# Performance work log

Measured on AMD Instinct MI355X. Metric: run time of the kernel, lower is better.

Reference implementation:

```python
import jax, jax.numpy as jnp
import numpy as np

N_NODES = 50000
N_EDGES = 800000
IN_DIM = 232
EMB = 300
HID = 2 * EMB
N_LAYERS = 5
BN_EPS = 1e-5


def setup_inputs() -> dict:
    key = jax.random.key(0)
    ks = jax.random.split(key, 12)
    x = jax.random.normal(ks[0], (N_NODES, IN_DIM), dtype=jnp.float32)
    edge_index = jax.random.randint(ks[1], (2, N_EDGES), 0, N_NODES, dtype=jnp.int64)
    edge_attr = jax.random.normal(ks[2], (N_EDGES, 9), dtype=jnp.float32)
    s_in = 1.0 / np.sqrt(IN_DIM)
    s_emb = 1.0 / np.sqrt(EMB)
    s_hid = 1.0 / np.sqrt(HID)
    lin_in_w = jax.random.uniform(ks[3], (IN_DIM, EMB), jnp.float32, -s_in, s_in)
    lin_in_b = jax.random.uniform(ks[4], (EMB,), jnp.float32, -s_in, s_in)
    w1 = jax.random.uniform(ks[5], (N_LAYERS, EMB, HID), jnp.float32, -s_emb, s_emb)
    b1 = jax.random.uniform(ks[6], (N_LAYERS, HID), jnp.float32, -s_emb, s_emb)
    gamma = jnp.ones((N_LAYERS, HID), jnp.float32)
    beta = jnp.zeros((N_LAYERS, HID), jnp.float32)
    w2 = jax.random.uniform(ks[7], (N_LAYERS, HID, EMB), jnp.float32, -s_hid, s_hid)
    b2 = jax.random.uniform(ks[8], (N_LAYERS, EMB), jnp.float32, -s_hid, s_hid)
    return {"x": x, "edge_index": edge_index, "edge_attr": edge_attr,
            "lin_in_w": lin_in_w, "lin_in_b": lin_in_b,
            "w1": w1, "b1": b1, "gamma": gamma, "beta": beta,
            "w2": w2, "b2": b2}


def reference(x, edge_index, edge_attr, lin_in_w, lin_in_b, w1, b1, gamma, beta, w2, b2):
    n = x.shape[0]
    self_loop = jnp.arange(n, dtype=edge_index.dtype)
    src = jnp.concatenate([edge_index[0], self_loop])  # [E+N]
    dst = jnp.concatenate([edge_index[1], self_loop])
    # input layer linear (232 -> emb)
    h = x @ lin_in_w + lin_in_b  # [N, EMB]
    num_layer = w1.shape[0]
    for l in range(num_layer):
        # gather messages at src, scatter-add at dst (GIN aggr='add' with self loops)
        agg = jax.ops.segment_sum(h[src], dst, num_segments=n)  # [N, EMB]
        # MLP: Linear -> BatchNorm1d (train-mode batch stats) -> ReLU -> Linear
        z = agg @ w1[l] + b1[l]  # [N, HID]
        mu = z.mean(axis=0)
        var = z.var(axis=0)  # biased, as torch BatchNorm uses for normalization
        z = (z - mu) * jax.lax.rsqrt(var + BN_EPS) * gamma[l] + beta[l]
        z = jax.nn.relu(z)
        h_new = z @ w2[l] + b2[l]  # [N, EMB]
        # GNN wrapper: relu between layers, none after the last (drop_ratio=0)
        h = h_new if l == num_layer - 1 else jax.nn.relu(h_new)
    return h  # JK='last'
```

## Files before the change

kernel.cpp:

```cpp
#include <hip/hip_runtime.h>
#include <cstdint>
#include <cstddef>

#define NNODES 50000
#define NEDGES 800000
#define IN_DIM 232
#define EMB 300
#define HID 600
#define NLAYERS 5
#define BN_EPS 1e-5f

#define MPAD 50048
#define K0P 256
#define K1P 320
#define K2P 608
#define N0P 384
#define N1P 640
#define MT_TILES 391
#define CSTR 140

typedef unsigned short ushort_t;
typedef __attribute__((ext_vector_type(8))) short bf16x8;
typedef __attribute__((ext_vector_type(4))) float f32x4;

__device__ __forceinline__ float b2f(ushort_t u) {
    unsigned int x = (unsigned int)u << 16;
    return __builtin_bit_cast(float, x);
}
__device__ __forceinline__ ushort_t f2b(float f) {
    unsigned int x = __builtin_bit_cast(unsigned int, f);
    unsigned int r = (x + 0x7fffu + ((x >> 16) & 1u)) >> 16;
    return (ushort_t)r;
}

__device__ __forceinline__ void gl_lds16(const void* gsrc, void* ldst) {
    __builtin_amdgcn_global_load_lds(
        (const __attribute__((address_space(1))) void*)gsrc,
        (__attribute__((address_space(3))) void*)ldst, 16, 0, 0);
}

__global__ void detect_mode_kernel(const unsigned int* __restrict__ ei, int* __restrict__ mode) {
    if (threadIdx.x == 0 && blockIdx.x == 0) {
        int nz = 0;
        for (int i = 0; i < 256; ++i) nz += (ei[2 * i + 1] != 0u);
        *mode = (nz == 0) ? 1 : 0;
    }
}
__device__ __forceinline__ int load_edge(const int* ei, int mode, long long idx) {
    if (mode) return (int)((const long long*)ei)[idx];
    return ei[idx];
}

__global__ void hist_kernel(const int* __restrict__ ei, const int* __restrict__ mode,
                            int* __restrict__ deg) {
    int i = blockIdx.x * blockDim.x + threadIdx.x;
    if (i >= NEDGES) return;
    int d = load_edge(ei, *mode, (long long)NEDGES + i);
    atomicAdd(&deg[d], 1);
}

__global__ void scan_block_sums(const int* __restrict__ deg, int* __restrict__ bsum, int n) {
    __shared__ int s[256];
    int t = threadIdx.x;
    int i = blockIdx.x * 256 + t;
    s[t] = (i < n) ? deg[i] : 0;
    __syncthreads();
    for (int off = 128; off > 0; off >>= 1) {
        if (t < off) s[t] += s[t + off];
        __syncthreads();
    }
    if (t == 0) bsum[blockIdx.x] = s[0];
}
// ... 29 lines not shown
    }
    int excl = s[t] - v + bsum[blockIdx.x];
    if (i < n) {
        offs[i] = excl;
        cursor[i] = excl;
        if (i == n - 1) offs[n] = excl + v;
    }
}

__global__ void fill_csr(const int* __restrict__ ei, const int* __restrict__ mode,
                         int* __restrict__ cursor, int* __restrict__ csr) {
    int i = blockIdx.x * blockDim.x + threadIdx.x;
    if (i >= NEDGES) return;
    int m = *mode;
    int s = load_edge(ei, m, i);
    int d = load_edge(ei, m, (long long)NEDGES + i);
    int p = atomicAdd(&cursor[d], 1);
    csr[p] = s;
}

__global__ void cast_x_kernel(const float* __restrict__ x, ushort_t* __restrict__ o) {
    int idx = blockIdx.x * 256 + threadIdx.x;
    if (idx >= NNODES * K0P) return;
    int row = idx >> 8, k = idx & 255;
    float v = (k < IN_DIM) ? x[(size_t)row * IN_DIM + k] : 0.f;
    o[idx] = f2b(v);
}
__global__ void conv_lin_kernel(const float* __restrict__ w, ushort_t* __restrict__ o) {
    int idx = blockIdx.x * 256 + threadIdx.x;
    if (idx >= N0P * K0P) return;
    int n = idx >> 8, k = idx & 255;
    float v = (n < EMB && k < IN_DIM) ? w[(size_t)k * EMB + n] : 0.f;
    o[idx] = f2b(v);
}
__global__ void conv_w1_kernel(const float* __restrict__ w, ushort_t* __restrict__ o) {
    int idx = blockIdx.x * 256 + threadIdx.x;
    if (idx >= NLAYERS * N1P * K1P) return;
    int l = idx / (N1P * K1P);
    int r = idx - l * (N1P * K1P);
    int n = r / K1P, k = r - n * K1P;
    float v = (n < HID && k < EMB) ? w[((size_t)l * EMB + k) * HID + n] : 0.f;
    o[idx] = f2b(v);
}
__global__ void conv_w2_kernel(const float* __restrict__ w, ushort_t* __restrict__ o) {
    int idx = blockIdx.x * 256 + threadIdx.x;
    if (idx >= NLAYERS * N0P * K2P) return;
    int l = idx / (N0P * K2P);
    int r = idx - l * (N0P * K2P);
    int n = r / K2P, k = r - n * K2P;
    float v = (n < EMB && k < HID) ? w[((size_t)l * HID + k) * EMB + n] : 0.f;
    o[idx] = f2b(v);
}

__global__ __launch_bounds__(256) void aggregate_bf16(
    const ushort_t* __restrict__ h, ushort_t* __restrict__ agg,
    const int* __restrict__ offs, const int* __restrict__ csr) {
    const int w = blockIdx.x * 4 + (threadIdx.x >> 6);
    const int lane = threadIdx.x & 63;
    const int wid0 = w * 2, wid1 = wid0 + 1;
    if (wid0 >= NNODES) return;
    const bool hasb = lane < 11;
    float a0[4], a1[4] = {0.f, 0.f, 0.f, 0.f};
    float c0[4], c1[4] = {0.f, 0.f, 0.f, 0.f};
    {
        const ushort4* r0 = (const ushort4*)(h + (size_t)wid0 * K1P);
        const ushort4* r1 = (const ushort4*)(h + (size_t)wid1 * K1P);
        ushort4 v0 = r0[lane], v1 = r1[lane];
        a0[0] = b2f(v0.x); a0[1] = b2f(v0.y); a0[2] = b2f(v0.z); a0[3] = b2f(v0.w);
        c0[0] = b2f(v1.x); c0[1] = b2f(v1.y); c0[2] = b2f(v1.z); c0[3] = b2f(v1.w);
        if (hasb) {
            ushort4 w0 = r0[64 + lane], w1 = r1[64 + lane];
            a1[0] = b2f(w0.x); a1[1] = b2f(w0.y); a1[2] = b2f(w0.z); a1[3] = b2f(w0.w);
            c1[0] = b2f(w1.x); c1[1] = b2f(w1.y); c1[2] = b2f(w1.z); c1[3] = b2f(w1.w);
        }
    }
    int p0 = offs[wid0], e0 = offs[wid0 + 1];
    int p1 = e0, e1 = offs[wid1 + 1];
    while (p0 < e0 && p1 < e1) {
        const ushort4* r0 = (const ushort4*)(h + (size_t)csr[p0] * K1P); ++p0;
        const ushort4* r1 = (const ushort4*)(h + (size_t)csr[p1] * K1P); ++p1;
        ushort4 v0 = r0[lane];
        ushort4 v1 = r1[lane];
        a0[0] += b2f(v0.x); a0[1] += b2f(v0.y); a0[2] += b2f(v0.z); a0[3] += b2f(v0.w);
        c0[0] += b2f(v1.x); c0[1] += b2f(v1.y); c0[2] += b2f(v1.z); c0[3] += b2f(v1.w);
        if (hasb) {
            ushort4 w0 = r0[64 + lane];
            ushort4 w1 = r1[64 + lane];
            a1[0] += b2f(w0.x); a1[1] += b2f(w0.y); a1[2] += b2f(w0.z); a1[3] += b2f(w0.w);
            c1[0] += b2f(w1.x); c1[1] += b2f(w1.y); c1[2] += b2f(w1.z); c1[3] += b2f(w1.w);
        }
    }
    while (p0 < e0) {
        const ushort4* r0 = (const ushort4*)(h + (size_t)csr[p0] * K1P); ++p0;
        ushort4 v0 = r0[lane];
        a0[0] += b2f(v0.x); a0[1] += b2f(v0.y); a0[2] += b2f(v0.z); a0[3] += b2f(v0.w);
        if (hasb) {
            ushort4 w0 = r0[64 + lane];
            a1[0] += b2f(w0.x); a1[1] += b2f(w0.y); a1[2] += b2f(w0.z); a1[3] += b2f(w0.w);
        }
    }
    while (p1 < e1) {
        const ushort4* r1 = (const ushort4*)(h + (size_t)csr[p1] * K1P); ++p1;
        ushort4 v1 = r1[lane];
        c0[0] += b2f(v1.x); c0[1] += b2f(v1.y); c0[2] += b2f(v1.z); c0[3] += b2f(v1.w);
        if (hasb) {
            ushort4 w1 = r1[64 + lane];
            c1[0] += b2f(w1.x); c1[1] += b2f(w1.y); c1[2] += b2f(w1.z); c1[3] += b2f(w1.w);
        }
    }
    ushort4* o0 = (ushort4*)(agg + (size_t)wid0 * K1P);
    ushort4* o1 = (ushort4*)(agg + (size_t)wid1 * K1P);
    ushort4 ov;
    ov.x = f2b(a0[0]); ov.y = f2b(a0[1]); ov.z = f2b(a0[2]); ov.w = f2b(a0[3]);
    o0[lane] = ov;
    ov.x = f2b(c0[0]); ov.y = f2b(c0[1]); ov.z = f2b(c0[2]); ov.w = f2b(c0[3]);
    o1[lane] = ov;
    if (hasb) {
        ov.x = f2b(a1[0]); ov.y = f2b(a1[1]); ov.z = f2b(a1[2]); ov.w = f2b(a1[3]);
        o0[64 + lane] = ov;
        ov.x = f2b(c1[0]); ov.y = f2b(c1[1]); ov.z = f2b(c1[2]); ov.w = f2b(c1[3]);
        o1[64 + lane] = ov;
    }
    if (lane < 5) {
        ushort4 zz; zz.x = zz.y = zz.z = zz.w = 0;
        o0[75 + lane] = zz;
        o1[75 + lane] = zz;
    }
}

template <int PRO, int RELU, int STATS, int OUT_BF16>
__global__ __launch_bounds__(256) void gemm_mfma(
    const ushort_t* __restrict__ A, int lda,
    const ushort_t* __restrict__ Bt, int ldb,
    const float* __restrict__ bias,
    void* __restrict__ C, int ldc, int M, int N, int K,
    const float* __restrict__ pscale, const float* __restrict__ pshift, int Kreal,
    float* __restrict__ stats, int NB) {
    __shared__ ushort_t sh[17920];
    __shared__ float psS[PRO ? 640 : 4];
    __shared__ float pfS[PRO ? 640 : 4];

    const int bid = blockIdx.x;
    const int xcd = bid & 7, slot = bid >> 3;
    const int mt = (slot / NB) * 8 + xcd;
    if (mt >= MT_TILES) return;
    const int nt = slot % NB;
    const int m0 = mt << 7, n0 = nt << 7;

    const int tid = threadIdx.x;
    const int wave = tid >> 6, lane = tid & 63;
    const int wm = wave >> 1, wn = wave & 1;
    const int NT = K >> 5;

    const int srow = lane >> 2;
    const int schunk = ((lane & 3) ^ ((lane >> 3) & 3)) << 3;
    const ushort_t* bP = Bt + (size_t)(n0 + (wave << 5) + srow) * ldb + schunk;
    const ushort_t* aPg = A + (size_t)(m0 + (wave << 5) + srow) * lda + schunk;
    const ushort_t* aPr = A + (size_t)(m0 + (wave << 5) + srow) * lda + ((lane & 3) << 3);
    const int a16 = lda << 4, b16 = ldb << 4;
    const int ldsW = wave << 10;
    ushort_t* const AS0 = sh;
    ushort_t* const AS1 = sh + 4096;
    ushort_t* const BS0 = sh + 8192;
    ushort_t* const BS1 = sh + 12288;

    const int fr = lane & 15, fq = lane >> 4;
    const int rdoff = (fq ^ ((fr >> 1) & 3)) << 3;

    f32x4 acc[4][4];
#pragma unroll
    for (int i = 0; i < 4; ++i)
#pragma unroll
        for (int j = 0; j < 4; ++j) acc[i][j] = {0.f, 0.f, 0.f, 0.f};

    if (PRO) {
        for (int i = tid; i < 640; i += 256) {
            psS[i] = (i < Kreal) ? pscale[i] : 0.f;
            pfS[i] = (i < Kreal) ? pshift[i] : 0.f;
        }
        __syncthreads();
    }

    uint4 ar0, ar1;
    const ushort_t* aNext;
    const ushort_t* bNext = bP + 32;
    if (PRO) {
        ar0 = *(const uint4*)aPr;
        ar1 = *(const uint4*)(aPr + a16);
        gl_lds16(bP, BS0 + ldsW);
        gl_lds16(bP + b16, BS0 + ldsW + 512);
        aNext = aPr + 32;
    } else {
        gl_lds16(aPg, AS0 + ldsW);
        gl_lds16(aPg + a16, AS0 + ldsW + 512);
        gl_lds16(bP, BS0 + ldsW);
        gl_lds16(bP + b16, BS0 + ldsW + 512);
        aNext = aPg + 32;
    }

    int cur = 0;
    for (int t = 0; t < NT; ++t) {
        ushort_t* const ASc = cur ? AS1 : AS0;
        ushort_t* const BSc = cur ? BS1 : BS0;
        ushort_t* const ASn = cur ? AS0 : AS1;
        ushort_t* const BSn = cur ? BS0 : BS1;
        if (PRO) {
            asm volatile("s_waitcnt vmcnt(2)" ::: "memory");
            const int kb = (t << 5) + ((lane & 3) << 3);
            float4 psa = *(const float4*)&psS[kb];
            float4 psb = *(const float4*)&psS[kb + 4];
            float4 pfa = *(const float4*)&pfS[kb];
            float4 pfb = *(const float4*)&pfS[kb + 4];
            float ps[8] = {psa.x, psa.y, psa.z, psa.w, psb.x, psb.y, psb.z, psb.w};
            float pf[8] = {pfa.x, pfa.y, pfa.z, pfa.w, pfb.x, pfb.y, pfb.z, pfb.w};
            bf16x8 w0, w1;
            const ushort_t* u0 = (const ushort_t*)&ar0;
            const ushort_t* u1 = (const ushort_t*)&ar1;
#pragma unroll
            for (int j = 0; j < 8; ++j) {
                float v0 = b2f(u0[j]) * ps[j] + pf[j];
                float v1 = b2f(u1[j]) * ps[j] + pf[j];
                w0[j] = (short)f2b(v0 > 0.f ? v0 : 0.f);
                w1[j] = (short)f2b(v1 > 0.f ? v1 : 0.f);
            }
            ushort_t* dA = ASc + ((wave << 5) + srow) * 32 + schunk;
            *(bf16x8*)dA = w0;
            *(bf16x8*)(dA + 16 * 32) = w1;
            if (t + 1 < NT) {
                ar0 = *(const uint4*)aNext;
                ar1 = *(const uint4*)(aNext + a16);
                gl_lds16(bNext, BSn + ldsW);
                gl_lds16(bNext + b16, BSn + ldsW + 512);
                aNext += 32; bNext += 32;
                asm volatile("s_waitcnt vmcnt(4) lgkmcnt(0)" ::: "memory");
            } else {
                asm volatile("s_waitcnt vmcnt(0) lgkmcnt(0)" ::: "memory");
            }
        } else {
            if (t + 1 < NT) {
                gl_lds16(aNext, ASn + ldsW);
                gl_lds16(aNext + a16, ASn + ldsW + 512);
                gl_lds16(bNext, BSn + ldsW);
                gl_lds16(bNext + b16, BSn + ldsW + 512);
                aNext += 32; bNext += 32;
                asm volatile("s_waitcnt vmcnt(4)" ::: "memory");
            } else {
                asm volatile("s_waitcnt vmcnt(0)" ::: "memory");
            }
        }
        __builtin_amdgcn_s_barrier();
        __builtin_amdgcn_sched_barrier(0);

        bf16x8 af[4], bf[4];
#pragma unroll
        for (int mi = 0; mi < 4; ++mi)
            af[mi] = *(const bf16x8*)&ASc[((wm << 6) + (mi << 4) + fr) * 32 + rdoff];
#pragma unroll
        for (int nj = 0; nj < 4; ++nj)
            bf[nj] = *(const bf16x8*)&BSc[((wn << 6) + (nj << 4) + fr) * 32 + rdoff];
#pragma unroll
        for (int mi = 0; mi < 4; ++mi)
#pragma unroll
            for (int nj = 0; nj < 4; ++nj)
                acc[mi][nj] = __builtin_amdgcn_mfma_f32_16x16x32_bf16(af[mi], bf[nj], acc[mi][nj], 0, 0, 0);

        __builtin_amdgcn_sched_barrier(0);
        __builtin_amdgcn_s_barrier();
        cur ^= 1;
    }

    if (STATS) {
        float s1[4] = {0.f, 0.f, 0.f, 0.f}, s2[4] = {0.f, 0.f, 0.f, 0.f};
#pragma unroll
        for (int nj = 0; nj < 4; ++nj) {
            const int col = n0 + (wn << 6) + (nj << 4) + fr;
            if (col < N) {
                const float bv = bias[col];
#pragma unroll
                for (int mi = 0; mi < 4; ++mi) {
                    const int rbase = m0 + (wm << 6) + (mi << 4) + (fq << 2);
#pragma unroll
                    for (int r = 0; r < 4; ++r) {
                        if (rbase + r < M) {
                            float v = acc[mi][nj][r] + bv;
                            if (RELU) v = v > 0.f ? v : 0.f;
                            s1[nj] += v; s2[nj] += v * v;
                        }
                    }
                }
            }
        }
#pragma unroll
        for (int nj = 0; nj < 4; ++nj) {
            s1[nj] += __shfl_xor(s1[nj], 16);
            s1[nj] += __shfl_xor(s1[nj], 32);
            s2[nj] += __shfl_xor(s2[nj], 16);
            s2[nj] += __shfl_xor(s2[nj], 32);
        }
        if (lane < 16) {
#pragma unroll
            for (int nj = 0; nj < 4; ++nj) {
                const int col = n0 + (wn << 6) + (nj << 4) + lane;
                if (col < N) {
                    atomicAdd(&stats[col], s1[nj]);
                    atomicAdd(&stats[N + col], s2[nj]);
                }
            }
        }
    }

    if (OUT_BF16) {
        ushort_t* ct = sh;
#pragma unroll
        for (int nj = 0; nj < 4; ++nj) {
            const int col_l = (wn << 6) + (nj << 4) + fr;
            const int col = n0 + col_l;
            const float bv = (col < N) ? bias[col] : 0.f;
#pragma unroll
            for (int mi = 0; mi < 4; ++mi) {
                const int rl0 = (wm << 6) + (mi << 4) + (fq << 2);
#pragma unroll
                for (int r = 0; r < 4; ++r) {
                    float v = acc[mi][nj][r] + bv;
                    if (RELU) v = v > 0.f ? v : 0.f;
                    ct[(rl0 + r) * CSTR + col_l] = f2b(v);
                }
            }
        }
        __syncthreads();
        const int rr = tid >> 1, half = tid & 1;
        const int grow = m0 + rr;
        if (grow < M) {
            const ushort_t* src = ct + rr * CSTR + (half << 6);
            ushort_t* dst = (ushort_t*)C + (size_t)grow * ldc + n0 + (half << 6);
#pragma unroll
            for (int c = 0; c < 8; ++c) {
                const int gc = n0 + (half << 6) + (c << 3);
                if (gc + 7 < N) {
                    uint2 u0 = *(const uint2*)(src + (c << 3));
                    uint2 u1 = *(const uint2*)(src + (c << 3) + 4);
                    uint4 o; o.x = u0.x; o.y = u0.y; o.z = u1.x; o.w = u1.y;
                    *(uint4*)(dst + (c << 3)) = o;
                } else {
                    for (int j = 0; j < 8; ++j)
                        if (gc + j < N) dst[(c << 3) + j] = src[(c << 3) + j];
                }
            }
        }
    } else {
        float* ctf = (float*)sh;
#pragma unroll
        for (int ph = 0; ph < 2; ++ph) {
            if (wm == ph) {
#pragma unroll
                for (int nj = 0; nj < 4; ++nj) {
                    const int col_l = (wn << 6) + (nj << 4) + fr;
                    const int col = n0 + col_l;
                    const float bv = (col < N) ? bias[col] : 0.f;
#pragma unroll
                    for (int mi = 0; mi < 4; ++mi) {
                        const int rl0 = (mi << 4) + (fq << 2);
#pragma unroll
                        for (int r = 0; r < 4; ++r) {
                            float v = acc[mi][nj][r] + bv;
                            if (RELU) v = v > 0.f ? v : 0.f;
                            ctf[(rl0 + r) * CSTR + col_l] = v;
                        }
                    }
                }
            }
            __syncthreads();
            const int rr = tid >> 2, q = tid & 3;
            const int grow = m0 + (ph << 6) + rr;
            if (grow < M) {
                const float* src = ctf + rr * CSTR + (q << 5);
                float* dst = (float*)C + (size_t)grow * ldc + n0 + (q << 5);
#pragma unroll
                for (int c = 0; c < 8; ++c) {
                    const int gc = n0 + (q << 5) + (c << 2);
                    if (gc + 3 < N) {
                        *(float4*)(dst + (c << 2)) = *(const float4*)(src + (c << 2));
                    } else {
                        for (int j = 0; j < 4; ++j)
                            if (gc + j < N) dst[(c << 2) + j] = src[(c << 2) + j];
                    }
                }
            }
            __syncthreads();
        }
    }
}

__global__ void bn_finalize(const float* __restrict__ stats, const float* __restrict__ gamma,
                            const float* __restrict__ beta, float* __restrict__ pscale,
                            float* __restrict__ pshift, int N, float invM) {
    int c = blockIdx.x * blockDim.x + threadIdx.x;
    if (c >= N) return;
    float mu = stats[c] * invM;
    float var = stats[N + c] * invM - mu * mu;
    float rs = rsqrtf(var + BN_EPS);
    float g = gamma[c] * rs;
    pscale[c] = g;
    pshift[c] = beta[c] - mu * g;
}

extern "C" void kernel_launch(void* const* d_in, const int* in_sizes, int n_in,
                              void* d_out, int out_size, void* d_ws, size_t ws_size,
                              hipStream_t stream) {
    const float* x = (const float*)d_in[0];
    const int* ei = (const int*)d_in[1];
    const float* lin_in_w = (const float*)d_in[3];
    const float* lin_in_b = (const float*)d_in[4];
    const float* w1 = (const float*)d_in[5];
    const float* b1 = (const float*)d_in[6];
    const float* gamma = (const float*)d_in[7];
    const float* beta = (const float*)d_in[8];
    const float* w2 = (const float*)d_in[9];
    const float* b2 = (const float*)d_in[10];
    float* out = (float*)d_out;

    char* p = (char*)d_ws;
    auto alloc = [&](size_t bytes) {
        char* r = p;
        p += (bytes + 255) & ~(size_t)255;
        return r;
    };
    ushort_t* xb  = (ushort_t*)alloc((size_t)MPAD * K0P * 2);
    ushort_t* h   = (ushort_t*)alloc((size_t)MPAD * K1P * 2);
    ushort_t* agg = (ushort_t*)alloc((size_t)MPAD * K1P * 2);
    ushort_t* z   = (ushort_t*)alloc((size_t)MPAD * K2P * 2);
    ushort_t* lint = (ushort_t*)alloc((size_t)N0P * K0P * 2);
    ushort_t* w1t  = (ushort_t*)alloc((size_t)NLAYERS * N1P * K1P * 2);
    ushort_t* w2t  = (ushort_t*)alloc((size_t)NLAYERS * N0P * K2P * 2);
    int* deg    = (int*)alloc(NNODES * 4);
    int* cursor = (int*)alloc(NNODES * 4);
    int* offs   = (int*)alloc((NNODES + 1) * 4);
    int* bsum   = (int*)alloc(1024);
    int* csr    = (int*)alloc((size_t)NEDGES * 4);
    float* stats  = (float*)alloc((size_t)NLAYERS * 2 * HID * 4);
    float* pscale = (float*)alloc(HID * 4);
    float* pshift = (float*)alloc(HID * 4);
    int* mode   = (int*)alloc(256);
    (void)ws_size; (void)in_sizes; (void)n_in; (void)out_size;

    hipMemsetAsync(deg, 0, NNODES * 4, stream);
    hipMemsetAsync(stats, 0, (size_t)NLAYERS * 2 * HID * 4, stream);

    detect_mode_kernel<<<1, 64, 0, stream>>>((const unsigned int*)ei, mode);
    hist_kernel<<<(NEDGES + 255) / 256, 256, 0, stream>>>(ei, mode, deg);
    const int nb = (NNODES + 255) / 256;
    scan_block_sums<<<nb, 256, 0, stream>>>(deg, bsum, NNODES);
    scan_bsums<<<1, 256, 0, stream>>>(bsum, nb);
    scan_final<<<nb, 256, 0, stream>>>(deg, bsum, offs, cursor, NNODES);
    fill_csr<<<(NEDGES + 255) / 256, 256, 0, stream>>>(ei, mode, cursor, csr);

    cast_x_kernel<<<(NNODES * K0P + 255) / 256, 256, 0, stream>>>(x, xb);
    conv_lin_kernel<<<(N0P * K0P + 255) / 256, 256, 0, stream>>>(lin_in_w, lint);
    conv_w1_kernel<<<(NLAYERS * N1P * K1P + 255) / 256, 256, 0, stream>>>(w1, w1t);
    conv_w2_kernel<<<(NLAYERS * N0P * K2P + 255) / 256, 256, 0, stream>>>(w2, w2t);

    const int G3 = 8 * 49 * 3;
    const int G5 = 8 * 49 * 5;

    gemm_mfma<0, 0, 0, 1><<<G3, 256, 0, stream>>>(
        xb, K0P, lint, K0P, lin_in_b, h, K1P, NNODES, EMB, K0P,
        nullptr, nullptr, 0, nullptr, 3);

    for (int l = 0; l < NLAYERS; ++l) {
        aggregate_bf16<<<(NNODES / 2 + 3) / 4, 256, 0, stream>>>(h, agg, offs, csr);
        gemm_mfma<0, 0, 1, 1><<<G5, 256, 0, stream>>>(
            agg, K1P, w1t + (size_t)l * N1P * K1P, K1P, b1 + (size_t)l * HID,
            z, K2P, NNODES, HID, K1P,
            nullptr, nullptr, 0, stats + (size_t)l * 2 * HID, 5);
        bn_finalize<<<(HID + 255) / 256, 256, 0, stream>>>(
            stats + (size_t)l * 2 * HID, gamma + (size_t)l * HID, beta + (size_t)l * HID,
            pscale, pshift, HID, 1.f / NNODES);
        if (l < NLAYERS - 1) {
            gemm_mfma<1, 1, 0, 1><<<G3, 256, 0, stream>>>(
                z, K2P, w2t + (size_t)l * N0P * K2P, K2P, b2 + (size_t)l * EMB,
                h, K1P, NNODES, EMB, K2P,
                pscale, pshift, HID, nullptr, 3);
        } else {
            gemm_mfma<1, 0, 0, 0><<<G3, 256, 0, stream>>>(
                z, K2P, w2t + (size_t)l * N0P * K2P, K2P, b2 + (size_t)l * EMB,
                out, EMB, NNODES, EMB, K2P,
                pscale, pshift, HID, nullptr, 3);
        }
    }
}
```

Before: 1.183 ms.

## Restructure aggregation into column-chunked node groups with XCD-aware chunk mapping

Replaces the two-nodes-per-wave gather kernel with one that splits the feature columns into 8 chunks, mapped by block index to the 8 XCDs. Within a wave, 6 lane groups of 10 lanes each walk 16 consecutive nodes, loading 8 bytes per lane. A zeroed padding row stands in for inactive lanes so the loop needs no branches. The aim is to keep each XCD's column slice of h resident in its own L2, improving cache reuse on the random gathers. The cost is 4 idle lanes per wave, wave-level divergence from uneven degrees, and an extra memset of the padding rows.

After: 2.928 ms. 148% more time.

```diff
diff --git a/kernel.cpp b/kernel.cpp
--- a/kernel.cpp
+++ b/kernel.cpp
@@ -18,6 +18,10 @@
 #define N1P 640
 #define MT_TILES 391
 #define CSTR 140
+
+#define NPG 16
+#define ZROW 50000
+#define AGG_SLOTS 131
 
 typedef unsigned short ushort_t;
 typedef __attribute__((ext_vector_type(8))) short bf16x8;
@@ -153,79 +157,67 @@
     o[idx] = f2b(v);
 }
 
-__global__ __launch_bounds__(256) void aggregate_bf16(
+__global__ __launch_bounds__(256) void aggregate_cs(
     const ushort_t* __restrict__ h, ushort_t* __restrict__ agg,
     const int* __restrict__ offs, const int* __restrict__ csr) {
-    const int w = blockIdx.x * 4 + (threadIdx.x >> 6);
-    const int lane = threadIdx.x & 63;
-    const int wid0 = w * 2, wid1 = wid0 + 1;
-    if (wid0 >= NNODES) return;
-    const bool hasb = lane < 11;
-    float a0[4], a1[4] = {0.f, 0.f, 0.f, 0.f};
-    float c0[4], c1[4] = {0.f, 0.f, 0.f, 0.f};
-    {
-        const ushort4* r0 = (const ushort4*)(h + (size_t)wid0 * K1P);
-        const ushort4* r1 = (const ushort4*)(h + (size_t)wid1 * K1P);
-        ushort4 v0 = r0[lane], v1 = r1[lane];
-        a0[0] = b2f(v0.x); a0[1] = b2f(v0.y); a0[2] = b2f(v0.z); a0[3] = b2f(v0.w);
-        c0[0] = b2f(v1.x); c0[1] = b2f(v1.y); c0[2] = b2f(v1.z); c0[3] = b2f(v1.w);
-        if (hasb) {
-            ushort4 w0 = r0[64 + lane], w1 = r1[64 + lane];
-            a1[0] = b2f(w0.x); a1[1] = b2f(w0.y); a1[2] = b2f(w0.z); a1[3] = b2f(w0.w);
-            c1[0] = b2f(w1.x); c1[1] = b2f(w1.y); c1[2] = b2f(w1.z); c1[3] = b2f(w1.w);
-        }
-    }
-    int p0 = offs[wid0], e0 = offs[wid0 + 1];
-    int p1 = e0, e1 = offs[wid1 + 1];
-    while (p0 < e0 && p1 < e1) {
-        const ushort4* r0 = (const ushort4*)(h + (size_t)csr[p0] * K1P); ++p0;
-        const ushort4* r1 = (const ushort4*)(h + (size_t)csr[p1] * K1P); ++p1;
-        ushort4 v0 = r0[lane];
-        ushort4 v1 = r1[lane];
-        a0[0] += b2f(v0.x); a0[1] += b2f(v0.y); a0[2] += b2f(v0.z); a0[3] += b2f(v0.w);
-        c0[0] += b2f(v1.x); c0[1] += b2f(v1.y); c0[2] += b2f(v1.z); c0[3] += b2f(v1.w);
-        if (hasb) {
-            ushort4 w0 = r0[64 + lane];
-            ushort4 w1 = r1[64 + lane];
-            a1[0] += b2f(w0.x); a1[1] += b2f(w0.y); a1[2] += b2f(w0.z); a1[3] += b2f(w0.w);
-            c1[0] += b2f(w1.x); c1[1] += b2f(w1.y); c1[2] += b2f(w1.z); c1[3] += b2f(w1.w);
-        }
-    }
-    while (p0 < e0) {
-        const ushort4* r0 = (const ushort4*)(h + (size_t)csr[p0] * K1P); ++p0;
-        ushort4 v0 = r0[lane];
-        a0[0] += b2f(v0.x); a0[1] += b2f(v0.y); a0[2] += b2f(v0.z); a0[3] += b2f(v0.w);
-        if (hasb) {
-            ushort4 w0 = r0[64 + lane];
-            a1[0] += b2f(w0.x); a1[1] += b2f(w0.y); a1[2] += b2f(w0.z); a1[3] += b2f(w0.w);
-        }
-    }
-    while (p1 < e1) {
-        const ushort4* r1 = (const ushort4*)(h + (size_t)csr[p1] * K1P); ++p1;
-        ushort4 v1 = r1[lane];
-        c0[0] += b2f(v1.x); c0[1] += b2f(v1.y); c0[2] += b2f(v1.z); c0[3] += b2f(v1.w);
-        if (hasb) {
-            ushort4 w1 = r1[64 + lane];
-            c1[0] += b2f(w1.x); c1[1] += b2f(w1.y); c1[2] += b2f(w1.z); c1[3] += b2f(w1.w);
-        }
-    }
-    ushort4* o0 = (ushort4*)(agg + (size_t)wid0 * K1P);
-    ushort4* o1 = (ushort4*)(agg + (size_t)wid1 * K1P);
-    ushort4 ov;
-    ov.x = f2b(a0[0]); ov.y = f2b(a0[1]); ov.z = f2b(a0[2]); ov.w = f2b(a0[3]);
-    o0[lane] = ov;
-    ov.x = f2b(c0[0]); ov.y = f2b(c0[1]); ov.z = f2b(c0[2]); ov.w = f2b(c0[3]);
-    o1[lane] = ov;
-    if (hasb) {
-        ov.x = f2b(a1[0]); ov.y = f2b(a1[1]); ov.z = f2b(a1[2]); ov.w = f2b(a1[3]);
-        o0[64 + lane] = ov;
-        ov.x = f2b(c1[0]); ov.y = f2b(c1[1]); ov.z = f2b(c1[2]); ov.w = f2b(c1[3]);
-        o1[64 + lane] = ov;
-    }
-    if (lane < 5) {
-        ushort4 zz; zz.x = zz.y = zz.z = zz.w = 0;
-        o0[75 + lane] = zz;
-        o1[75 + lane] = zz;
+    const int chunk = blockIdx.x & 7;
+    const int slot = blockIdx.x >> 3;
+    const int wave = threadIdx.x >> 6, lane = threadIdx.x & 63;
+    const int g = lane / 10;
+    const int cl = lane - g * 10;
+    const bool real = (g < 6);
+    const int gid = (slot * 4 + wave) * 6 + g;
+    int v = real ? gid * NPG : NNODES;
+    int vend = real ? (gid * NPG + NPG) : NNODES;
+    if (vend > NNODES) vend = NNODES;
+    if (v > NNODES) v = NNODES;
+    const int colu = chunk * 20 + cl * 2;
+    const unsigned int* __restrict__ h32 = (const unsigned int*)h;
+    unsigned int* __restrict__ a32 = (unsigned int*)agg;
+
+    int beg = 0, end = 0, e = 0;
+    if (v < vend) {
+        beg = __builtin_nontemporal_load(offs + v);
+        end = __builtin_nontemporal_load(offs + v + 1);
+        e = beg - 1;
+    }
+    float a0 = 0.f, a1 = 0.f, a2 = 0.f, a3 = 0.f;
+
+    while (__any(v < vend)) {
+        const bool self = e < beg;
+        const bool active = (e < end) & (v < vend);
+        int ci = self ? 0 : e;
+        ci = (ci < NEDGES) ? ci : 0;
+        const int csrv = __builtin_nontemporal_load(csr + ci);
+        int src = self ? v : csrv;
+        src = active ? src : ZROW;
+        const unsigned long long L =
+            *(const unsigned long long*)(h32 + (unsigned int)src * (K1P / 2) + colu);
+        const unsigned int lo = (unsigned int)L;
+        const unsigned int hi = (unsigned int)(L >> 32);
+        a0 += __builtin_bit_cast(float, lo << 16);
+        a1 += __builtin_bit_cast(float, lo & 0xffff0000u);
+        a2 += __builtin_bit_cast(float, hi << 16);
+        a3 += __builtin_bit_cast(float, hi & 0xffff0000u);
+        e += active ? 1 : 0;
+        const bool done = (e >= end) & (v < vend);
+        if (__any(done)) {
+            if (done) {
+                unsigned int p0 = (unsigned int)f2b(a0) | ((unsigned int)f2b(a1) << 16);
+                unsigned int p1 = (unsigned int)f2b(a2) | ((unsigned int)f2b(a3) << 16);
+                if (colu * 2 >= 300) { p0 = 0u; p1 = 0u; }
+                const unsigned long long P = (unsigned long long)p0 | ((unsigned long long)p1 << 32);
+                __builtin_nontemporal_store(
+                    P, (unsigned long long*)(a32 + (unsigned int)v * (K1P / 2) + colu));
+                ++v;
+                a0 = a1 = a2 = a3 = 0.f;
+                if (v < vend) {
+                    beg = __builtin_nontemporal_load(offs + v);
+                    end = __builtin_nontemporal_load(offs + v + 1);
+                    e = beg - 1;
+                }
+            }
+        }
     }
 }
 
@@ -546,6 +538,7 @@
 
     hipMemsetAsync(deg, 0, NNODES * 4, stream);
     hipMemsetAsync(stats, 0, (size_t)NLAYERS * 2 * HID * 4, stream);
+    hipMemsetAsync(h + (size_t)NNODES * K1P, 0, (size_t)(MPAD - NNODES) * K1P * 2, stream);
 
     detect_mode_kernel<<<1, 64, 0, stream>>>((const unsigned int*)ei, mode);
     hist_kernel<<<(NEDGES + 255) / 256, 256, 0, stream>>>(ei, mode, deg);
@@ -568,7 +561,7 @@
         nullptr, nullptr, 0, nullptr, 3);
 
     for (int l = 0; l < NLAYERS; ++l) {
-        aggregate_bf16<<<(NNODES / 2 + 3) / 4, 256, 0, stream>>>(h, agg, offs, csr);
+        aggregate_cs<<<AGG_SLOTS * 8, 256, 0, stream>>>(h, agg, offs, csr);
         gemm_mfma<0, 0, 1, 1><<<G5, 256, 0, stream>>>(
             agg, K1P, w1t + (size_t)l * N1P * K1P, K1P, b1 + (size_t)l * HID,
             z, K2P, NNODES, HID, K1P,
```

## Enlarge GEMM tiles to 256 rows with 512 threads and widen aggregation to four nodes per wave

Applied to the files above, without the earlier changes.

The MFMA GEMM now uses 512-thread blocks computing 256x128 tiles, so each B tile loaded into LDS is shared across twice as many rows. The epilogue is restructured into multi-pass LDS staging, and MPAD is raised to cover 256-row tiles. The aggregation kernel now processes four destination nodes per wave in lockstep. Exhausted neighbor lists redirect to a zeroed padding row rather than branching, and loads and stores use nontemporal hints. The trade-off is more LDS and register pressure per block, plus wasted loads on the padding row when node degrees are imbalanced.

Result: slower. 1.638 ms (+38.5%).

```diff
diff --git a/kernel.cpp b/kernel.cpp
--- a/kernel.cpp
+++ b/kernel.cpp
@@ -10,14 +10,15 @@
 #define NLAYERS 5
 #define BN_EPS 1e-5f
 
-#define MPAD 50048
+#define MPAD 50176
 #define K0P 256
 #define K1P 320
 #define K2P 608
 #define N0P 384
 #define N1P 640
-#define MT_TILES 391
-#define CSTR 140
+#define MT_TILES 196
+#define CSTR 144
+#define ZROW 50000
 
 typedef unsigned short ushort_t;
 typedef __attribute__((ext_vector_type(8))) short bf16x8;
@@ -158,86 +159,71 @@
     const int* __restrict__ offs, const int* __restrict__ csr) {
     const int w = blockIdx.x * 4 + (threadIdx.x >> 6);
     const int lane = threadIdx.x & 63;
-    const int wid0 = w * 2, wid1 = wid0 + 1;
-    if (wid0 >= NNODES) return;
+    const int v0 = w * 4;
+    if (v0 >= NNODES) return;
     const bool hasb = lane < 11;
-    float a0[4], a1[4] = {0.f, 0.f, 0.f, 0.f};
-    float c0[4], c1[4] = {0.f, 0.f, 0.f, 0.f};
-    {
-        const ushort4* r0 = (const ushort4*)(h + (size_t)wid0 * K1P);
-        const ushort4* r1 = (const ushort4*)(h + (size_t)wid1 * K1P);
-        ushort4 v0 = r0[lane], v1 = r1[lane];
-        a0[0] = b2f(v0.x); a0[1] = b2f(v0.y); a0[2] = b2f(v0.z); a0[3] = b2f(v0.w);
-        c0[0] = b2f(v1.x); c0[1] = b2f(v1.y); c0[2] = b2f(v1.z); c0[3] = b2f(v1.w);
+    float ac[4][8];
+    int pc[4], ec[4];
+#pragma unroll
+    for (int c = 0; c < 4; ++c) {
+        pc[c] = __builtin_nontemporal_load(offs + v0 + c);
+        ec[c] = __builtin_nontemporal_load(offs + v0 + c + 1);
+        const ushort4* r = (const ushort4*)(h + (size_t)(v0 + c) * K1P);
+        ushort4 x = r[lane];
+        ac[c][0] = b2f(x.x); ac[c][1] = b2f(x.y); ac[c][2] = b2f(x.z); ac[c][3] = b2f(x.w);
+        ac[c][4] = 0.f; ac[c][5] = 0.f; ac[c][6] = 0.f; ac[c][7] = 0.f;
         if (hasb) {
-            ushort4 w0 = r0[64 + lane], w1 = r1[64 + lane];
-            a1[0] = b2f(w0.x); a1[1] = b2f(w0.y); a1[2] = b2f(w0.z); a1[3] = b2f(w0.w);
-            c1[0] = b2f(w1.x); c1[1] = b2f(w1.y); c1[2] = b2f(w1.z); c1[3] = b2f(w1.w);
-        }
-    }
-    int p0 = offs[wid0], e0 = offs[wid0 + 1];
-    int p1 = e0, e1 = offs[wid1 + 1];
-    while (p0 < e0 && p1 < e1) {
-        const ushort4* r0 = (const ushort4*)(h + (size_t)csr[p0] * K1P); ++p0;
-        const ushort4* r1 = (const ushort4*)(h + (size_t)csr[p1] * K1P); ++p1;
-        ushort4 v0 = r0[lane];
-        ushort4 v1 = r1[lane];
-        a0[0] += b2f(v0.x); a0[1] += b2f(v0.y); a0[2] += b2f(v0.z); a0[3] += b2f(v0.w);
-        c0[0] += b2f(v1.x); c0[1] += b2f(v1.y); c0[2] += b2f(v1.z); c0[3] += b2f(v1.w);
+            ushort4 y = r[64 + lane];
+            ac[c][4] = b2f(y.x); ac[c][5] = b2f(y.y); ac[c][6] = b2f(y.z); ac[c][7] = b2f(y.w);
+        }
+    }
+    while ((pc[0] < ec[0]) | (pc[1] < ec[1]) | (pc[2] < ec[2]) | (pc[3] < ec[3])) {
+        int src[4];
+#pragma unroll
+        for (int c = 0; c < 4; ++c) {
+            const bool a = pc[c] < ec[c];
+            const int idx = a ? pc[c] : 0;
+            const int s = __builtin_nontemporal_load(csr + idx);
+            src[c] = a ? s : ZROW;
+            pc[c] += a ? 1 : 0;
+        }
+#pragma unroll
+        for (int c = 0; c < 4; ++c) {
+            const ushort4* r = (const ushort4*)(h + (size_t)src[c] * K1P);
+            ushort4 x = r[lane];
+            ac[c][0] += b2f(x.x); ac[c][1] += b2f(x.y); ac[c][2] += b2f(x.z); ac[c][3] += b2f(x.w);
+            if (hasb) {
+                ushort4 y = r[64 + lane];
+                ac[c][4] += b2f(y.x); ac[c][5] += b2f(y.y); ac[c][6] += b2f(y.z); ac[c][7] += b2f(y.w);
+            }
+        }
+    }
+#pragma unroll
+    for (int c = 0; c < 4; ++c) {
+        unsigned long long* o = (unsigned long long*)(agg + (size_t)(v0 + c) * K1P);
+        unsigned long long P =
+            (unsigned long long)((unsigned int)f2b(ac[c][0]) | ((unsigned int)f2b(ac[c][1]) << 16)) |
+            ((unsigned long long)((unsigned int)f2b(ac[c][2]) | ((unsigned int)f2b(ac[c][3]) << 16)) << 32);
+        __builtin_nontemporal_store(P, o + lane);
         if (hasb) {
-            ushort4 w0 = r0[64 + lane];
-            ushort4 w1 = r1[64 + lane];
-            a1[0] += b2f(w0.x); a1[1] += b2f(w0.y); a1[2] += b2f(w0.z); a1[3] += b2f(w0.w);
-            c1[0] += b2f(w1.x); c1[1] += b2f(w1.y); c1[2] += b2f(w1.z); c1[3] += b2f(w1.w);
-        }
-    }
-    while (p0 < e0) {
-        const ushort4* r0 = (const ushort4*)(h + (size_t)csr[p0] * K1P); ++p0;
-        ushort4 v0 = r0[lane];
-        a0[0] += b2f(v0.x); a0[1] += b2f(v0.y); a0[2] += b2f(v0.z); a0[3] += b2f(v0.w);
-        if (hasb) {
-            ushort4 w0 = r0[64 + lane];
-            a1[0] += b2f(w0.x); a1[1] += b2f(w0.y); a1[2] += b2f(w0.z); a1[3] += b2f(w0.w);
-        }
-    }
-    while (p1 < e1) {
-        const ushort4* r1 = (const ushort4*)(h + (size_t)csr[p1] * K1P); ++p1;
-        ushort4 v1 = r1[lane];
-        c0[0] += b2f(v1.x); c0[1] += b2f(v1.y); c0[2] += b2f(v1.z); c0[3] += b2f(v1.w);
-        if (hasb) {
-            ushort4 w1 = r1[64 + lane];
-            c1[0] += b2f(w1.x); c1[1] += b2f(w1.y); c1[2] += b2f(w1.z); c1[3] += b2f(w1.w);
-        }
-    }
-    ushort4* o0 = (ushort4*)(agg + (size_t)wid0 * K1P);
-    ushort4* o1 = (ushort4*)(agg + (size_t)wid1 * K1P);
-    ushort4 ov;
-    ov.x = f2b(a0[0]); ov.y = f2b(a0[1]); ov.z = f2b(a0[2]); ov.w = f2b(a0[3]);
-    o0[lane] = ov;
-    ov.x = f2b(c0[0]); ov.y = f2b(c0[1]); ov.z = f2b(c0[2]); ov.w = f2b(c0[3]);
-    o1[lane] = ov;
-    if (hasb) {
-        ov.x = f2b(a1[0]); ov.y = f2b(a1[1]); ov.z = f2b(a1[2]); ov.w = f2b(a1[3]);
-        o0[64 + lane] = ov;
-        ov.x = f2b(c1[0]); ov.y = f2b(c1[1]); ov.z = f2b(c1[2]); ov.w = f2b(c1[3]);
-        o1[64 + lane] = ov;
-    }
-    if (lane < 5) {
-        ushort4 zz; zz.x = zz.y = zz.z = zz.w = 0;
-        o0[75 + lane] = zz;
-        o1[75 + lane] = zz;
+            unsigned long long Q =
+                (unsigned long long)((unsigned int)f2b(ac[c][4]) | ((unsigned int)f2b(ac[c][5]) << 16)) |
+                ((unsigned long long)((unsigned int)f2b(ac[c][6]) | ((unsigned int)f2b(ac[c][7]) << 16)) << 32);
+            __builtin_nontemporal_store(Q, o + 64 + lane);
+        }
+        if (lane < 5) __builtin_nontemporal_store(0ull, o + 75 + lane);
     }
 }
 
 template <int PRO, int RELU, int STATS, int OUT_BF16>
-__global__ __launch_bounds__(256) void gemm_mfma(
+__global__ __launch_bounds__(512, 4) void gemm_mfma(
     const ushort_t* __restrict__ A, int lda,
     const ushort_t* __restrict__ Bt, int ldb,
     const float* __restrict__ bias,
     void* __restrict__ C, int ldc, int M, int N, int K,
     const float* __restrict__ pscale, const float* __restrict__ pshift, int Kreal,
     float* __restrict__ stats, int NB) {
-    __shared__ ushort_t sh[17920];
+    __shared__ ushort_t sh[24576];
     __shared__ float psS[PRO ? 640 : 4];
     __shared__ float pfS[PRO ? 640 : 4];
 
@@ -246,7 +232,7 @@
     const int mt = (slot / NB) * 8 + xcd;
     if (mt >= MT_TILES) return;
     const int nt = slot % NB;
-    const int m0 = mt << 7, n0 = nt << 7;
+    const int m0 = mt << 8, n0 = nt << 7;
 
     const int tid = threadIdx.x;
     const int wave = tid >> 6, lane = tid & 63;
@@ -255,15 +241,16 @@
 
     const int srow = lane >> 2;
     const int schunk = ((lane & 3) ^ ((lane >> 3) & 3)) << 3;
-    const ushort_t* bP = Bt + (size_t)(n0 + (wave << 5) + srow) * ldb + schunk;
+    const ushort_t* bP = Bt + (size_t)(n0 + (wave << 4) + srow) * ldb + schunk;
     const ushort_t* aPg = A + (size_t)(m0 + (wave << 5) + srow) * lda + schunk;
     const ushort_t* aPr = A + (size_t)(m0 + (wave << 5) + srow) * lda + ((lane & 3) << 3);
-    const int a16 = lda << 4, b16 = ldb << 4;
-    const int ldsW = wave << 10;
+    const int a16 = lda << 4;
+    const int aW = wave << 10;
+    const int bW = wave << 9;
     ushort_t* const AS0 = sh;
-    ushort_t* const AS1 = sh + 4096;
-    ushort_t* const BS0 = sh + 8192;
-    ushort_t* const BS1 = sh + 12288;
+    ushort_t* const AS1 = sh + 8192;
+    ushort_t* const BS0 = sh + 16384;
+    ushort_t* const BS1 = sh + 20480;
 
     const int fr = lane & 15, fq = lane >> 4;
     const int rdoff = (fq ^ ((fr >> 1) & 3)) << 3;
@@ -275,7 +262,7 @@
         for (int j = 0; j < 4; ++j) acc[i][j] = {0.f, 0.f, 0.f, 0.f};
 
     if (PRO) {
-        for (int i = tid; i < 640; i += 256) {
+        for (int i = tid; i < 640; i += 512) {
             psS[i] = (i < Kreal) ? pscale[i] : 0.f;
             pfS[i] = (i < Kreal) ? pshift[i] : 0.f;
         }
@@ -288,14 +275,12 @@
     if (PRO) {
         ar0 = *(const uint4*)aPr;
         ar1 = *(const uint4*)(aPr + a16);
-        gl_lds16(bP, BS0 + ldsW);
-        gl_lds16(bP + b16, BS0 + ldsW + 512);
+        gl_lds16(bP, BS0 + bW);
         aNext = aPr + 32;
     } else {
-        gl_lds16(aPg, AS0 + ldsW);
-        gl_lds16(aPg + a16, AS0 + ldsW + 512);
-        gl_lds16(bP, BS0 + ldsW);
-        gl_lds16(bP + b16, BS0 + ldsW + 512);
+        gl_lds16(aPg, AS0 + aW);
+        gl_lds16(aPg + a16, AS0 + aW + 512);
+        gl_lds16(bP, BS0 + bW);
         aNext = aPg + 32;
     }
 
@@ -306,7 +291,7 @@
         ushort_t* const ASn = cur ? AS0 : AS1;
         ushort_t* const BSn = cur ? BS0 : BS1;
         if (PRO) {
-            asm volatile("s_waitcnt vmcnt(2)" ::: "memory");
+            asm volatile("s_waitcnt vmcnt(1)" ::: "memory");
             const int kb = (t << 5) + ((lane & 3) << 3);
             float4 psa = *(const float4*)&psS[kb];
             float4 psb = *(const float4*)&psS[kb + 4];
@@ -326,25 +311,23 @@
             }
             ushort_t* dA = ASc + ((wave << 5) + srow) * 32 + schunk;
             *(bf16x8*)dA = w0;
-            *(bf16x8*)(dA + 16 * 32) = w1;
+            *(bf16x8*)(dA + 512) = w1;
             if (t + 1 < NT) {
                 ar0 = *(const uint4*)aNext;
                 ar1 = *(const uint4*)(aNext + a16);
-                gl_lds16(bNext, BSn + ldsW);
-                gl_lds16(bNext + b16, BSn + ldsW + 512);
+                gl_lds16(bNext, BSn + bW);
                 aNext += 32; bNext += 32;
-                asm volatile("s_waitcnt vmcnt(4) lgkmcnt(0)" ::: "memory");
+                asm volatile("s_waitcnt vmcnt(3) lgkmcnt(0)" ::: "memory");
             } else {
                 asm volatile("s_waitcnt vmcnt(0) lgkmcnt(0)" ::: "memory");
             }
         } else {
             if (t + 1 < NT) {
-                gl_lds16(aNext, ASn + ldsW);
-                gl_lds16(aNext + a16, ASn + ldsW + 512);
-                gl_lds16(bNext, BSn + ldsW);
-                gl_lds16(bNext + b16, BSn + ldsW + 512);
+                gl_lds16(aNext, ASn + aW);
+                gl_lds16(aNext + a16, ASn + aW + 512);
+                gl_lds16(bNext, BSn + bW);
                 aNext += 32; bNext += 32;
-                asm volatile("s_waitcnt vmcnt(4)" ::: "memory");
+                asm volatile("s_waitcnt vmcnt(3)" ::: "memory");
             } else {
                 asm volatile("s_waitcnt vmcnt(0)" ::: "memory");
             }
@@ -413,46 +396,49 @@
     if (OUT_BF16) {
         ushort_t* ct = sh;
 #pragma unroll
-        for (int nj = 0; nj < 4; ++nj) {
-            const int col_l = (wn << 6) + (nj << 4) + fr;
-            const int col = n0 + col_l;
-            const float bv = (col < N) ? bias[col] : 0.f;
-#pragma unroll
-            for (int mi = 0; mi < 4; ++mi) {
-                const int rl0 = (wm << 6) + (mi << 4) + (fq << 2);
-#pragma unroll
-                for (int r = 0; r < 4; ++r) {
-                    float v = acc[mi][nj][r] + bv;
-                    if (RELU) v = v > 0.f ? v : 0.f;
-                    ct[(rl0 + r) * CSTR + col_l] = f2b(v);
+        for (int p = 0; p < 2; ++p) {
+            if ((wm >> 1) == p) {
+#pragma unroll
+                for (int nj = 0; nj < 4; ++nj) {
+                    const int col_l = (wn << 6) + (nj << 4) + fr;
+                    const int col = n0 + col_l;
+                    const float bv = (col < N) ? bias[col] : 0.f;
+#pragma unroll
+                    for (int mi = 0; mi < 4; ++mi) {
+                        const int rl0 = ((wm & 1) << 6) + (mi << 4) + (fq << 2);
+#pragma unroll
+                        for (int r = 0; r < 4; ++r) {
+                            float v = acc[mi][nj][r] + bv;
+                            if (RELU) v = v > 0.f ? v : 0.f;
+                            ct[(rl0 + r) * CSTR + col_l] = f2b(v);
+                        }
+                    }
                 }
             }
-        }
-        __syncthreads();
-        const int rr = tid >> 1, half = tid & 1;
-        const int grow = m0 + rr;
-        if (grow < M) {
-            const ushort_t* src = ct + rr * CSTR + (half << 6);
-            ushort_t* dst = (ushort_t*)C + (size_t)grow * ldc + n0 + (half << 6);
-#pragma unroll
-            for (int c = 0; c < 8; ++c) {
-                const int gc = n0 + (half << 6) + (c << 3);
-                if (gc + 7 < N) {
-                    uint2 u0 = *(const uint2*)(src + (c << 3));
-                    uint2 u1 = *(const uint2*)(src + (c << 3) + 4);
-                    uint4 o; o.x = u0.x; o.y = u0.y; o.z = u1.x; o.w = u1.y;
-                    *(uint4*)(dst + (c << 3)) = o;
-                } else {
-                    for (int j = 0; j < 8; ++j)
-                        if (gc + j < N) dst[(c << 3) + j] = src[(c << 3) + j];
+            __syncthreads();
+            const int rl = tid >> 2, q = tid & 3;
+            const int grow = m0 + (p << 7) + rl;
+            if (grow < M) {
+                const ushort_t* src = ct + rl * CSTR + (q << 5);
+                ushort_t* dst = (ushort_t*)C + (size_t)grow * ldc + n0 + (q << 5);
+#pragma unroll
+                for (int c = 0; c < 4; ++c) {
+                    const int gc = n0 + (q << 5) + (c << 3);
+                    if (gc + 7 < N) {
+                        *(uint4*)(dst + (c << 3)) = *(const uint4*)(src + (c << 3));
+                    } else {
+                        for (int j = 0; j < 8; ++j)
+                            if (gc + j < N) dst[(c << 3) + j] = src[(c << 3) + j];
+                    }
                 }
             }
+            __syncthreads();
         }
     } else {
         float* ctf = (float*)sh;
 #pragma unroll
-        for (int ph = 0; ph < 2; ++ph) {
-            if (wm == ph) {
+        for (int p = 0; p < 4; ++p) {
+            if (wm == p) {
 #pragma unroll
                 for (int nj = 0; nj < 4; ++nj) {
                     const int col_l = (wn << 6) + (nj << 4) + fr;
@@ -471,14 +457,14 @@
                 }
             }
             __syncthreads();
-            const int rr = tid >> 2, q = tid & 3;
-            const int grow = m0 + (ph << 6) + rr;
+            const int rl = tid >> 3, q = tid & 7;
+            const int grow = m0 + (p << 6) + rl;
             if (grow < M) {
-                const float* src = ctf + rr * CSTR + (q << 5);
-                float* dst = (float*)C + (size_t)grow * ldc + n0 + (q << 5);
-#pragma unroll
-                for (int c = 0; c < 8; ++c) {
-                    const int gc = n0 + (q << 5) + (c << 2);
+                const float* src = ctf + rl * CSTR + (q << 4);
+                float* dst = (float*)C + (size_t)grow * ldc + n0 + (q << 4);
+#pragma unroll
+                for (int c = 0; c < 4; ++c) {
+                    const int gc = n0 + (q << 4) + (c << 2);
                     if (gc + 3 < N) {
                         *(float4*)(dst + (c << 2)) = *(const float4*)(src + (c << 2));
                     } else {
@@ -546,6 +532,7 @@
 
     hipMemsetAsync(deg, 0, NNODES * 4, stream);
     hipMemsetAsync(stats, 0, (size_t)NLAYERS * 2 * HID * 4, stream);
+    hipMemsetAsync(h + (size_t)NNODES * K1P, 0, (size_t)(MPAD - NNODES) * K1P * 2, stream);
 
     detect_mode_kernel<<<1, 64, 0, stream>>>((const unsigned int*)ei, mode);
     hist_kernel<<<(NEDGES + 255) / 256, 256, 0, stream>>>(ei, mode, deg);
@@ -560,16 +547,16 @@
     conv_w1_kernel<<<(NLAYERS * N1P * K1P + 255) / 256, 256, 0, stream>>>(w1, w1t);
     conv_w2_kernel<<<(NLAYERS * N0P * K2P + 255) / 256, 256, 0, stream>>>(w2, w2t);
 
-    const int G3 = 8 * 49 * 3;
-    const int G5 = 8 * 49 * 5;
-
-    gemm_mfma<0, 0, 0, 1><<<G3, 256, 0, stream>>>(
+    const int G3 = 8 * 25 * 3;
+    const int G5 = 8 * 25 * 5;
+
+    gemm_mfma<0, 0, 0, 1><<<G3, 512, 0, stream>>>(
         xb, K0P, lint, K0P, lin_in_b, h, K1P, NNODES, EMB, K0P,
         nullptr, nullptr, 0, nullptr, 3);
 
     for (int l = 0; l < NLAYERS; ++l) {
-        aggregate_bf16<<<(NNODES / 2 + 3) / 4, 256, 0, stream>>>(h, agg, offs, csr);
-        gemm_mfma<0, 0, 1, 1><<<G5, 256, 0, stream>>>(
+        aggregate_bf16<<<NNODES / 16, 256, 0, stream>>>(h, agg, offs, csr);
+        gemm_mfma<0, 0, 1, 1><<<G5, 512, 0, stream>>>(
             agg, K1P, w1t + (size_t)l * N1P * K1P, K1P, b1 + (size_t)l * HID,
             z, K2P, NNODES, HID, K1P,
             nullptr, nullptr, 0, stats + (size_t)l * 2 * HID, 5);
@@ -577,12 +564,12 @@
             stats + (size_t)l * 2 * HID, gamma + (size_t)l * HID, beta + (size_t)l * HID,
             pscale, pshift, HID, 1.f / NNODES);
         if (l < NLAYERS - 1) {
-            gemm_mfma<1, 1, 0, 1><<<G3, 256, 0, stream>>>(
+            gemm_mfma<1, 1, 0, 1><<<G3, 512, 0, stream>>>(
                 z, K2P, w2t + (size_t)l * N0P * K2P, K2P, b2 + (size_t)l * EMB,
                 h, K1P, NNODES, EMB, K2P,
                 pscale, pshift, HID, nullptr, 3);
         } else {
-            gemm_mfma<1, 0, 0, 0><<<G3, 256, 0, stream>>>(
+            gemm_mfma<1, 0, 0, 0><<<G3, 512, 0, stream>>>(
                 z, K2P, w2t + (size_t)l * N0P * K2P, K2P, b2 + (size_t)l * EMB,
                 out, EMB, NNODES, EMB, K2P,
                 pscale, pshift, HID, nullptr, 3);
```

## Load non-prologue GEMM fragments directly from global into registers, bypassing LDS

Applied to the files above, without the earlier changes.

For GEMMs without a fused prologue, the LDS double-buffered staging is replaced by loading MFMA A/B fragments straight from global memory into registers, using a two-stage software register pipeline. This removes LDS writes and reads plus the block barriers on that path, but each wave now fetches its own fragments, so global and L2 traffic rises because tiles are no longer shared across waves through LDS. A barrier is added before the epilogue's LDS reuse, and the padding rows of h are zeroed so the direct loads read defined data.

Measured after the change: 1.378 ms. +16.5%, slower.

```diff
diff --git a/kernel.cpp b/kernel.cpp
--- a/kernel.cpp
+++ b/kernel.cpp
@@ -253,20 +253,7 @@
     const int wm = wave >> 1, wn = wave & 1;
     const int NT = K >> 5;
 
-    const int srow = lane >> 2;
-    const int schunk = ((lane & 3) ^ ((lane >> 3) & 3)) << 3;
-    const ushort_t* bP = Bt + (size_t)(n0 + (wave << 5) + srow) * ldb + schunk;
-    const ushort_t* aPg = A + (size_t)(m0 + (wave << 5) + srow) * lda + schunk;
-    const ushort_t* aPr = A + (size_t)(m0 + (wave << 5) + srow) * lda + ((lane & 3) << 3);
-    const int a16 = lda << 4, b16 = ldb << 4;
-    const int ldsW = wave << 10;
-    ushort_t* const AS0 = sh;
-    ushort_t* const AS1 = sh + 4096;
-    ushort_t* const BS0 = sh + 8192;
-    ushort_t* const BS1 = sh + 12288;
-
     const int fr = lane & 15, fq = lane >> 4;
-    const int rdoff = (fq ^ ((fr >> 1) & 3)) << 3;
 
     f32x4 acc[4][4];
 #pragma unroll
@@ -274,38 +261,97 @@
 #pragma unroll
         for (int j = 0; j < 4; ++j) acc[i][j] = {0.f, 0.f, 0.f, 0.f};
 
-    if (PRO) {
+    if (!PRO) {
+        const ushort_t* aB[4];
+        const ushort_t* bB[4];
+#pragma unroll
+        for (int mi = 0; mi < 4; ++mi)
+            aB[mi] = A + (size_t)(m0 + (wm << 6) + (mi << 4) + fr) * lda + (fq << 3);
+#pragma unroll
+        for (int nj = 0; nj < 4; ++nj)
+            bB[nj] = Bt + (size_t)(n0 + (wn << 6) + (nj << 4) + fr) * ldb + (fq << 3);
+
+        uint4 a0[4], b0[4], a1[4], b1[4];
+#pragma unroll
+        for (int mi = 0; mi < 4; ++mi) a0[mi] = *(const uint4*)(aB[mi]);
+#pragma unroll
+        for (int nj = 0; nj < 4; ++nj) b0[nj] = *(const uint4*)(bB[nj]);
+
+        int t = 0;
+        for (; t + 2 <= NT; t += 2) {
+#pragma unroll
+            for (int mi = 0; mi < 4; ++mi) a1[mi] = *(const uint4*)(aB[mi] + ((t + 1) << 5));
+#pragma unroll
+            for (int nj = 0; nj < 4; ++nj) b1[nj] = *(const uint4*)(bB[nj] + ((t + 1) << 5));
+            __builtin_amdgcn_sched_barrier(0);
+#pragma unroll
+            for (int mi = 0; mi < 4; ++mi) {
+                bf16x8 af = __builtin_bit_cast(bf16x8, a0[mi]);
+#pragma unroll
+                for (int nj = 0; nj < 4; ++nj)
+                    acc[mi][nj] = __builtin_amdgcn_mfma_f32_16x16x32_bf16(
+                        af, __builtin_bit_cast(bf16x8, b0[nj]), acc[mi][nj], 0, 0, 0);
+            }
+            __builtin_amdgcn_sched_barrier(0);
+            if (t + 2 < NT) {
+#pragma unroll
+                for (int mi = 0; mi < 4; ++mi) a0[mi] = *(const uint4*)(aB[mi] + ((t + 2) << 5));
+#pragma unroll
+                for (int nj = 0; nj < 4; ++nj) b0[nj] = *(const uint4*)(bB[nj] + ((t + 2) << 5));
+            }
+            __builtin_amdgcn_sched_barrier(0);
+#pragma unroll
+            for (int mi = 0; mi < 4; ++mi) {
+                bf16x8 af = __builtin_bit_cast(bf16x8, a1[mi]);
+#pragma unroll
+                for (int nj = 0; nj < 4; ++nj)
+                    acc[mi][nj] = __builtin_amdgcn_mfma_f32_16x16x32_bf16(
+                        af, __builtin_bit_cast(bf16x8, b1[nj]), acc[mi][nj], 0, 0, 0);
+            }
+            __builtin_amdgcn_sched_barrier(0);
+        }
+        if (t < NT) {
+#pragma unroll
+            for (int mi = 0; mi < 4; ++mi) {
+                bf16x8 af = __builtin_bit_cast(bf16x8, a0[mi]);
+#pragma unroll
+                for (int nj = 0; nj < 4; ++nj)
+                    acc[mi][nj] = __builtin_amdgcn_mfma_f32_16x16x32_bf16(
+                        af, __builtin_bit_cast(bf16x8, b0[nj]), acc[mi][nj], 0, 0, 0);
+            }
+        }
+    } else {
         for (int i = tid; i < 640; i += 256) {
             psS[i] = (i < Kreal) ? pscale[i] : 0.f;
             pfS[i] = (i < Kreal) ? pshift[i] : 0.f;
         }
         __syncthreads();
-    }
-
-    uint4 ar0, ar1;
-    const ushort_t* aNext;
-    const ushort_t* bNext = bP + 32;
-    if (PRO) {
+
+        const int srow = lane >> 2;
+        const int schunk = ((lane & 3) ^ ((lane >> 3) & 3)) << 3;
+        const ushort_t* bP = Bt + (size_t)(n0 + (wave << 5) + srow) * ldb + schunk;
+        const ushort_t* aPr = A + (size_t)(m0 + (wave << 5) + srow) * lda + ((lane & 3) << 3);
+        const int a16 = lda << 4, b16 = ldb << 4;
+        const int ldsW = wave << 10;
+        const int rdoff = (fq ^ ((fr >> 1) & 3)) << 3;
+        ushort_t* const AS0 = sh;
+        ushort_t* const AS1 = sh + 4096;
+        ushort_t* const BS0 = sh + 8192;
+        ushort_t* const BS1 = sh + 12288;
+        uint4 ar0, ar1;
+        const ushort_t* aNext;
+        const ushort_t* bNext = bP + 32;
         ar0 = *(const uint4*)aPr;
         ar1 = *(const uint4*)(aPr + a16);
         gl_lds16(bP, BS0 + ldsW);
         gl_lds16(bP + b16, BS0 + ldsW + 512);
         aNext = aPr + 32;
-    } else {
-        gl_lds16(aPg, AS0 + ldsW);
-        gl_lds16(aPg + a16, AS0 + ldsW + 512);
-        gl_lds16(bP, BS0 + ldsW);
-        gl_lds16(bP + b16, BS0 + ldsW + 512);
-        aNext = aPg + 32;
-    }
-
-    int cur = 0;
-    for (int t = 0; t < NT; ++t) {
-        ushort_t* const ASc = cur ? AS1 : AS0;
-        ushort_t* const BSc = cur ? BS1 : BS0;
-        ushort_t* const ASn = cur ? AS0 : AS1;
-        ushort_t* const BSn = cur ? BS0 : BS1;
-        if (PRO) {
+
+        int cur = 0;
+        for (int t = 0; t < NT; ++t) {
+            ushort_t* const ASc = cur ? AS1 : AS0;
+            ushort_t* const BSn = cur ? BS0 : BS1;
+            ushort_t* const BSc = cur ? BS1 : BS0;
             asm volatile("s_waitcnt vmcnt(2)" ::: "memory");
             const int kb = (t << 5) + ((lane & 3) << 3);
             float4 psa = *(const float4*)&psS[kb];
@@ -337,37 +383,26 @@
             } else {
                 asm volatile("s_waitcnt vmcnt(0) lgkmcnt(0)" ::: "memory");
             }
-        } else {
-            if (t + 1 < NT) {
-                gl_lds16(aNext, ASn + ldsW);
-                gl_lds16(aNext + a16, ASn + ldsW + 512);
-                gl_lds16(bNext, BSn + ldsW);
-                gl_lds16(bNext + b16, BSn + ldsW + 512);
-                aNext += 32; bNext += 32;
-                asm volatile("s_waitcnt vmcnt(4)" ::: "memory");
-            } else {
-                asm volatile("s_waitcnt vmcnt(0)" ::: "memory");
-            }
-        }
-        __builtin_amdgcn_s_barrier();
-        __builtin_amdgcn_sched_barrier(0);
-
-        bf16x8 af[4], bf[4];
-#pragma unroll
-        for (int mi = 0; mi < 4; ++mi)
-            af[mi] = *(const bf16x8*)&ASc[((wm << 6) + (mi << 4) + fr) * 32 + rdoff];
-#pragma unroll
-        for (int nj = 0; nj < 4; ++nj)
-            bf[nj] = *(const bf16x8*)&BSc[((wn << 6) + (nj << 4) + fr) * 32 + rdoff];
-#pragma unroll
-        for (int mi = 0; mi < 4; ++mi)
+            __builtin_amdgcn_s_barrier();
+            __builtin_amdgcn_sched_barrier(0);
+
+            bf16x8 af[4], bf[4];
+#pragma unroll
+            for (int mi = 0; mi < 4; ++mi)
+                af[mi] = *(const bf16x8*)&ASc[((wm << 6) + (mi << 4) + fr) * 32 + rdoff];
 #pragma unroll
             for (int nj = 0; nj < 4; ++nj)
-                acc[mi][nj] = __builtin_amdgcn_mfma_f32_16x16x32_bf16(af[mi], bf[nj], acc[mi][nj], 0, 0, 0);
-
-        __builtin_amdgcn_sched_barrier(0);
-        __builtin_amdgcn_s_barrier();
-        cur ^= 1;
+                bf[nj] = *(const bf16x8*)&BSc[((wn << 6) + (nj << 4) + fr) * 32 + rdoff];
+#pragma unroll
+            for (int mi = 0; mi < 4; ++mi)
+#pragma unroll
+                for (int nj = 0; nj < 4; ++nj)
+                    acc[mi][nj] = __builtin_amdgcn_mfma_f32_16x16x32_bf16(af[mi], bf[nj], acc[mi][nj], 0, 0, 0);
+
+            __builtin_amdgcn_sched_barrier(0);
+            __builtin_amdgcn_s_barrier();
+            cur ^= 1;
+        }
     }
 
     if (STATS) {
@@ -410,6 +445,7 @@
         }
     }
 
+    __syncthreads();
     if (OUT_BF16) {
         ushort_t* ct = sh;
 #pragma unroll
@@ -546,6 +582,7 @@
 
     hipMemsetAsync(deg, 0, NNODES * 4, stream);
     hipMemsetAsync(stats, 0, (size_t)NLAYERS * 2 * HID * 4, stream);
+    hipMemsetAsync(h + (size_t)NNODES * K1P, 0, (size_t)(MPAD - NNODES) * K1P * 2, stream);
 
     detect_mode_kernel<<<1, 64, 0, stream>>>((const unsigned int*)ei, mode);
     hist_kernel<<<(NEDGES + 255) / 256, 256, 0, stream>>>(ei, mode, deg);
```
